# Optimization experiments

Measured on AMD Instinct MI355X. Metric: run time of the kernel, lower is better.

## Reference

```python
import jax, jax.numpy as jnp
import numpy as np

N_NODES = 50000


def sage_conv(x, src, dst, W_l, W_r, b):
    # mean-aggregate neighbor features: out_i = W_l @ mean_{j->i} x_j + W_r @ x_i + b
    msg_sum = jax.ops.segment_sum(x[src], dst, num_segments=N_NODES)   # [N, F]
    cnt = jax.ops.segment_sum(jnp.ones_like(dst, dtype=x.dtype), dst, num_segments=N_NODES)
    mean = msg_sum / jnp.maximum(cnt, 1.0)[:, None]                    # zero for isolated nodes
    return mean @ W_l + x @ W_r + b


def setup_inputs() -> dict:
    key = jax.random.key(0)
    ks = jax.random.split(key, 8)
    in_dim, hid, out_dim = 128, 128, 128
    x = jax.random.normal(ks[0], (N_NODES, in_dim), dtype=jnp.float32)
    edge_index = jax.random.randint(ks[1], (2, 800000), 0, N_NODES, dtype=jnp.int64)
    s0 = 1.0 / np.sqrt(in_dim)
    s1 = 1.0 / np.sqrt(hid)
    return {
        "x": x,
        "edge_index": edge_index,
        "W_l0": jax.random.uniform(ks[2], (in_dim, hid), jnp.float32, -s0, s0),
        "W_r0": jax.random.uniform(ks[3], (in_dim, hid), jnp.float32, -s0, s0),
        "b0": jnp.zeros((hid,), jnp.float32),
        "W_l1": jax.random.uniform(ks[4], (hid, out_dim), jnp.float32, -s1, s1),
        "W_r1": jax.random.uniform(ks[5], (hid, out_dim), jnp.float32, -s1, s1),
        "b1": jnp.zeros((out_dim,), jnp.float32),
    }


def reference(x, edge_index, W_l0, W_r0, b0, W_l1, W_r1, b1):
    src, dst = edge_index[0], edge_index[1]
    h = sage_conv(x, src, dst, W_l0, W_r0, b0)
    h = jax.nn.relu(h)
    out = sage_conv(h, src, dst, W_l1, W_r1, b1)
    return out
```

## Files before the change

### kernel.cpp

```cpp
#include <hip/hip_runtime.h>

#define FDIM 128

typedef __attribute__((ext_vector_type(4))) float f32x4;
typedef __attribute__((ext_vector_type(8))) short s16x8;
typedef __attribute__((ext_vector_type(4))) short s16x4;

__device__ inline unsigned short f2bf(float f) {
    unsigned u = __builtin_bit_cast(unsigned, f);
    u += 0x7FFFu + ((u >> 16) & 1u);
    return (unsigned short)(u >> 16);
}

__global__ void hist_kernel(const int* __restrict__ dst, int* __restrict__ deg, int E) {
    int e = blockIdx.x * blockDim.x + threadIdx.x;
    if (e < E) atomicAdd(&deg[dst[e]], 1);
}

__global__ void scan1_kernel(const int* __restrict__ deg, int* __restrict__ rp,
                             int* __restrict__ bsum, int N) {
    __shared__ int s[256];
    int i = blockIdx.x * 256 + threadIdx.x;
    int v = (i < N) ? deg[i] : 0;
    s[threadIdx.x] = v;
    __syncthreads();
    for (int off = 1; off < 256; off <<= 1) {
        int t = (threadIdx.x >= off) ? s[threadIdx.x - off] : 0;
        __syncthreads();
        s[threadIdx.x] += t;
        __syncthreads();
    }
    if (i < N) rp[i] = s[threadIdx.x] - v;
    if (threadIdx.x == 255) bsum[blockIdx.x] = s[255];
}

__global__ void scan2_kernel(int* __restrict__ bsum, int nb) {
    __shared__ int s[256];
    int v = (threadIdx.x < (unsigned)nb) ? bsum[threadIdx.x] : 0;
    s[threadIdx.x] = v;
    __syncthreads();
    for (int off = 1; off < 256; off <<= 1) {
        int t = (threadIdx.x >= off) ? s[threadIdx.x - off] : 0;
        __syncthreads();
        s[threadIdx.x] += t;
        __syncthreads();
    }
    if (threadIdx.x < (unsigned)nb) bsum[threadIdx.x] = s[threadIdx.x] - v;
}

__global__ void scan3_kernel(int* __restrict__ rp, const int* __restrict__ bsum,
                             int* __restrict__ cursor, int N, int E) {
    int i = blockIdx.x * 256 + threadIdx.x;
    if (i < N) {
        int v = rp[i] + bsum[blockIdx.x];
        rp[i] = v;
        cursor[i] = v;
    } else if (i == N) {
        rp[N] = E;
    }
}

__global__ void fill_kernel(const int* __restrict__ src, const int* __restrict__ dst,
                            int* __restrict__ cursor, int* __restrict__ eid, int E) {
    int e = blockIdx.x * blockDim.x + threadIdx.x;
    if (e < E) {
        int p = atomicAdd(&cursor[dst[e]], 1);
        eid[p] = src[e];
    }
}

__global__ void prep_x_kernel(const float* __restrict__ x, short* __restrict__ xb, int n4) {
    int i = blockIdx.x * blockDim.x + threadIdx.x;
    if (i < n4) {
        float4 v = reinterpret_cast<const float4*>(x)[i];
        s16x4 o;
        o[0] = (short)f2bf(v.x); o[1] = (short)f2bf(v.y);
        o[2] = (short)f2bf(v.z); o[3] = (short)f2bf(v.w);
        reinterpret_cast<s16x4*>(xb)[i] = o;
    }
}

__global__ void prep_w_kernel(const float* __restrict__ Wl0, const float* __restrict__ Wr0,
                              const float* __restrict__ Wl1, const float* __restrict__ Wr1,
                              short* __restrict__ Wt0, short* __restrict__ Wt1) {
    int g = blockIdx.x * blockDim.x + threadIdx.x;
    int n = g & 127;
    int k = (g >> 7) & 255;
    int layer = g >> 15;
    const float* Wl = layer ? Wl1 : Wl0;
    const float* Wr = layer ? Wr1 : Wr0;
    short* Wt = layer ? Wt1 : Wt0;
    float v = (k < 128) ? Wl[k * 128 + n] : Wr[(k - 128) * 128 + n];
    Wt[n * 256 + k] = (short)f2bf(v);
}

__global__ void gather_kernel(const short* __restrict__ xb, const int* __restrict__ rp,
                              const int* __restrict__ eid, short* __restrict__ mb, int N) {
    int node = blockIdx.x * (blockDim.x >> 6) + (threadIdx.x >> 6);
    int lane = threadIdx.x & 63;
    if (node >= N) return;
    int beg = rp[node], end = rp[node + 1];
    float ax = 0.f, ay = 0.f;
    int k = beg;
    for (; k + 4 <= end; k += 4) {
        int s0 = eid[k], s1 = eid[k + 1], s2 = eid[k + 2], s3 = eid[k + 3];
        unsigned u0 = reinterpret_cast<const unsigned*>(xb + (size_t)s0 * FDIM)[lane];
        unsigned u1 = reinterpret_cast<const unsigned*>(xb + (size_t)s1 * FDIM)[lane];
        unsigned u2 = reinterpret_cast<const unsigned*>(xb + (size_t)s2 * FDIM)[lane];
        unsigned u3 = reinterpret_cast<const unsigned*>(xb + (size_t)s3 * FDIM)[lane];
        ax += __builtin_bit_cast(float, u0 << 16) + __builtin_bit_cast(float, u1 << 16)
            + __builtin_bit_cast(float, u2 << 16) + __builtin_bit_cast(float, u3 << 16);
        ay += __builtin_bit_cast(float, u0 & 0xFFFF0000u) + __builtin_bit_cast(float, u1 & 0xFFFF0000u)
            + __builtin_bit_cast(float, u2 & 0xFFFF0000u) + __builtin_bit_cast(float, u3 & 0xFFFF0000u);
    }
    for (; k < end; ++k) {
        int s = eid[k];
        unsigned u = reinterpret_cast<const unsigned*>(xb + (size_t)s * FDIM)[lane];
        ax += __builtin_bit_cast(float, u << 16);
        ay += __builtin_bit_cast(float, u & 0xFFFF0000u);
    }
    float inv = (end > beg) ? 1.0f / (float)(end - beg) : 0.0f;
    unsigned lo = f2bf(ax * inv), hi = f2bf(ay * inv);
    reinterpret_cast<unsigned*>(mb + (size_t)node * FDIM)[lane] = lo | (hi << 16);
}

template <bool RELU, bool OUTF32>
__global__ __launch_bounds__(256, 2)
void gemm_mfma_kernel(const short* __restrict__ Am, const short* Ax,
                      const short* __restrict__ Wt, const float* __restrict__ bias,
                      float* outf, short* outb, int n) {
    __shared__ short A_lds[64 * 256];
    const int tid = threadIdx.x;
    const int w = tid >> 6, l = tid & 63;
    const int row0 = blockIdx.x * 64;

    s16x8 bfr[8][2];
    {
        const short* wb = Wt + ((32 * w + (l & 15)) * 256 + 8 * (l >> 4));
#pragma unroll
        for (int kc = 0; kc < 8; ++kc)
#pragma unroll
            for (int cf = 0; cf < 2; ++cf)
                bfr[kc][cf] = *reinterpret_cast<const s16x8*>(wb + cf * 16 * 256 + kc * 32);
    }

#pragma unroll
    for (int i = 0; i < 8; ++i) {
        int c = tid + 256 * i;
        int r = c >> 5;
        int ck = c & 31;
        int row = row0 + r;
        s16x8 v;
        if (row < n) {
            const short* sp = (ck < 16) ? (Am + (size_t)row * FDIM + ck * 8)
                                        : (Ax + (size_t)row * FDIM + (ck - 16) * 8);
            v = *reinterpret_cast<const s16x8*>(sp);
        } else {
#pragma unroll
            for (int j = 0; j < 8; ++j) v[j] = 0;
        }
        int byte = r * 512 + ((ck * 16) ^ ((r & 7) << 4));
        *reinterpret_cast<s16x8*>(reinterpret_cast<char*>(A_lds) + byte) = v;
    }
    __syncthreads();

    f32x4 acc[4][2];
    {
        float b0 = bias[32 * w + (l & 15)];
        float b1 = bias[32 * w + 16 + (l & 15)];
#pragma unroll
        for (int rf = 0; rf < 4; ++rf)
#pragma unroll
            for (int i = 0; i < 4; ++i) { acc[rf][0][i] = b0; acc[rf][1][i] = b1; }
    }

    const int arow = l & 15;
    const int aq16 = 16 * (l >> 4);
#pragma unroll
    for (int kc = 0; kc < 8; ++kc) {
        s16x8 afr[4];
#pragma unroll
        for (int rf = 0; rf < 4; ++rf) {
            int r = 16 * rf + arow;
            int kbyte = 64 * kc + aq16;
            int byte = r * 512 + (kbyte ^ ((r & 7) << 4));
            afr[rf] = *reinterpret_cast<const s16x8*>(reinterpret_cast<const char*>(A_lds) + byte);
        }
#pragma unroll
        for (int rf = 0; rf < 4; ++rf)
#pragma unroll
            for (int cf = 0; cf < 2; ++cf)
                acc[rf][cf] = __builtin_amdgcn_mfma_f32_16x16x32_bf16(afr[rf], bfr[kc][cf], acc[rf][cf], 0, 0, 0);
    }

    const int ocol = 32 * w + (l & 15);
    const int orow = 4 * (l >> 4);
#pragma unroll
    for (int rf = 0; rf < 4; ++rf)
#pragma unroll
        for (int cf = 0; cf < 2; ++cf)
#pragma unroll
            for (int i = 0; i < 4; ++i) {
                int row = row0 + 16 * rf + orow + i;
                if (row < n) {
                    float v = acc[rf][cf][i];
                    if (RELU) v = fmaxf(v, 0.0f);
                    if (OUTF32) outf[(size_t)row * FDIM + ocol + 16 * cf] = v;
                    else        outb[(size_t)row * FDIM + ocol + 16 * cf] = (short)f2bf(v);
                }
            }
}

__global__ void degree_kernel(const int* __restrict__ dst, float* __restrict__ cnt, int E) {
    int e = blockIdx.x * blockDim.x + threadIdx.x;
    if (e < E) atomicAdd(&cnt[dst[e]], 1.0f);
}

__global__ void scatter_kernel(const float* __restrict__ x, const int* __restrict__ src,
                               const int* __restrict__ dst, float* __restrict__ msg, int E) {
    int gt = blockIdx.x * blockDim.x + threadIdx.x;
    int e = gt >> 6;
    int lane = gt & 63;
    if (e >= E) return;
    int s = src[e];
    int d = dst[e];
    float2 v = reinterpret_cast<const float2*>(x + (size_t)s * FDIM)[lane];
    float* md = msg + (size_t)d * FDIM + 2 * lane;
    atomicAdd(md, v.x);
    atomicAdd(md + 1, v.y);
}

template <bool RELU>
__global__ void gemm_kernel(const float* agg, const float* cnt,
                            const float* __restrict__ xin, const float* __restrict__ Wl,
                            const float* __restrict__ Wr, const float* __restrict__ bias,
                            float* out, int n) {
    const int ROWS = 16;
    __shared__ float m_s[ROWS][FDIM];
    __shared__ float x_s[ROWS][FDIM];
    int tid = threadIdx.x;
    int row0 = blockIdx.x * ROWS;
#pragma unroll
    for (int i = 0; i < 2; ++i) {
        int idx4 = tid + i * 256;
        int r = idx4 >> 5;
        int c4 = idx4 & 31;
        int row = row0 + r;
        if (row < n) {
            float inv = cnt ? 1.0f / fmaxf(cnt[row], 1.0f) : 1.0f;
            float4 mv = reinterpret_cast<const float4*>(agg + (size_t)row * FDIM)[c4];
            float4 xv = reinterpret_cast<const float4*>(xin + (size_t)row * FDIM)[c4];
            float* mp = &m_s[r][c4 * 4];
            mp[0] = mv.x * inv; mp[1] = mv.y * inv; mp[2] = mv.z * inv; mp[3] = mv.w * inv;
            float* xp = &x_s[r][c4 * 4];
            xp[0] = xv.x; xp[1] = xv.y; xp[2] = xv.z; xp[3] = xv.w;
        }
    }
    __syncthreads();
    int j = tid & 127;
    int rh = tid >> 7;
    float acc[8];
    float bj = bias[j];
#pragma unroll
    for (int r = 0; r < 8; ++r) acc[r] = bj;
#pragma unroll 4
    for (int k = 0; k < FDIM; ++k) {
        float wl = Wl[k * FDIM + j];
        float wr = Wr[k * FDIM + j];
#pragma unroll
        for (int r = 0; r < 8; ++r)
            acc[r] += m_s[rh * 8 + r][k] * wl + x_s[rh * 8 + r][k] * wr;
    }
#pragma unroll
    for (int r = 0; r < 8; ++r) {
        int row = row0 + rh * 8 + r;
        if (row < n) {
            float v = acc[r];
            if (RELU) v = fmaxf(v, 0.0f);
            out[(size_t)row * FDIM + j] = v;
        }
    }
}

extern "C" void kernel_launch(void* const* d_in, const int* in_sizes, int n_in,
                              void* d_out, int out_size, void* d_ws, size_t ws_size,
                              hipStream_t stream) {
    const float* x   = (const float*)d_in[0];
    const int*   ei  = (const int*)d_in[1];
    const float* Wl0 = (const float*)d_in[2];
    const float* Wr0 = (const float*)d_in[3];
    const float* b0  = (const float*)d_in[4];
    const float* Wl1 = (const float*)d_in[5];
    const float* Wr1 = (const float*)d_in[6];
    const float* b1  = (const float*)d_in[7];

    int N = in_sizes[0] / FDIM;
    int E = in_sizes[1] / 2;
    const int* src = ei;
    const int* dst = ei + E;

    size_t featBytes  = (size_t)N * FDIM * sizeof(float);
    size_t featBytesB = (size_t)N * FDIM * sizeof(short);
    int edgeBlocks = (E + 255) / 256;
    int nb = (N + 255) / 256;

    const size_t o_deg  = 0;
    const size_t o_rp   = 0x40000;
    const size_t o_cur  = 0x80000;
    const size_t o_bsum = 0xC0000;
    const size_t o_wt0  = 0xD0000;
    const size_t o_wt1  = 0xE0000;
    const size_t o_eid  = 0x100000;
    const size_t o_xb   = 0x440000;
    const size_t o_mb   = o_xb + featBytesB;
    const size_t need   = o_mb + featBytesB;

    if (ws_size >= need) {
        int*   deg    = (int*)((char*)d_ws + o_deg);
        int*   rp     = (int*)((char*)d_ws + o_rp);
        int*   cursor = (int*)((char*)d_ws + o_cur);
        int*   bsum   = (int*)((char*)d_ws + o_bsum);
        short* Wt0    = (short*)((char*)d_ws + o_wt0);
        short* Wt1    = (short*)((char*)d_ws + o_wt1);
        int*   eid    = (int*)((char*)d_ws + o_eid);
        short* xb     = (short*)((char*)d_ws + o_xb);
        short* mb     = (short*)((char*)d_ws + o_mb);
        float* outF   = (float*)d_out;

        hipMemsetAsync(deg, 0, (size_t)N * sizeof(int), stream);
        hist_kernel<<<edgeBlocks, 256, 0, stream>>>(dst, deg, E);
        scan1_kernel<<<nb, 256, 0, stream>>>(deg, rp, bsum, N);
        scan2_kernel<<<1, 256, 0, stream>>>(bsum, nb);
        scan3_kernel<<<(N + 256) / 256, 256, 0, stream>>>(rp, bsum, cursor, N, E);
        fill_kernel<<<edgeBlocks, 256, 0, stream>>>(src, dst, cursor, eid, E);

        prep_w_kernel<<<256, 256, 0, stream>>>(Wl0, Wr0, Wl1, Wr1, Wt0, Wt1);
        prep_x_kernel<<<(N * FDIM / 4 + 255) / 256, 256, 0, stream>>>(x, xb, N * FDIM / 4);

        int gatherBlocks = (N + 3) / 4;
        int gemmBlocks   = (N + 63) / 64;
        gather_kernel<<<gatherBlocks, 256, 0, stream>>>(xb, rp, eid, mb, N);
        gemm_mfma_kernel<true, false><<<gemmBlocks, 256, 0, stream>>>(mb, xb, Wt0, b0, nullptr, xb, N);
        gather_kernel<<<gatherBlocks, 256, 0, stream>>>(xb, rp, eid, mb, N);
        gemm_mfma_kernel<false, true><<<gemmBlocks, 256, 0, stream>>>(mb, xb, Wt1, b1, outF, nullptr, N);
    } else {
        float* cnt = (float*)d_ws;
        float* h   = (float*)((char*)d_ws + (1 << 18));
        float* msg = (float*)d_out;
        int gemmBlocks = (N + 15) / 16;

        hipMemsetAsync(cnt, 0, (size_t)N * sizeof(float), stream);
        degree_kernel<<<edgeBlocks, 256, 0, stream>>>(dst, cnt, E);

        hipMemsetAsync(msg, 0, featBytes, stream);
        scatter_kernel<<<(E * 64 + 255) / 256, 256, 0, stream>>>(x, src, dst, msg, E);
        gemm_kernel<true><<<gemmBlocks, 256, 0, stream>>>(msg, cnt, x, Wl0, Wr0, b0, h, N);

        hipMemsetAsync(msg, 0, featBytes, stream);
        scatter_kernel<<<(E * 64 + 255) / 256, 256, 0, stream>>>(h, src, dst, msg, E);
        gemm_kernel<false><<<gemmBlocks, 256, 0, stream>>>(msg, cnt, h, Wl1, Wr1, b1, msg, N);
    }
}
```

Before: 218.0 us.

## Fuse neighbor mean-gather into MFMA GEMM kernel, writing aggregates directly to LDS

Merges the separate gather and GEMM kernels per layer into one kernel. Each wave gathers 16 rows of neighbor means straight into the swizzled LDS A tile, next to the self features, and then runs the MFMA GEMM. This removes the intermediate mean buffer round trip through global memory and two launches per layer, and it unrolls the gather by 8 for more loads in flight. A separate output buffer is now used for layer 1 because the kernel reads X for neighbors. In exchange, only 4 waves per 64 rows do the latency-bound gather, with fewer blocks than the old gather launch. Occupancy is raised to 3 blocks/SM via launch bounds to compensate.

```diff
diff --git a/kernel.cpp b/kernel.cpp
--- a/kernel.cpp
+++ b/kernel.cpp
@@ -11,6 +11,8 @@
     u += 0x7FFFu + ((u >> 16) & 1u);
     return (unsigned short)(u >> 16);
 }
+__device__ inline float bflo(unsigned u) { return __builtin_bit_cast(float, u << 16); }
+__device__ inline float bfhi(unsigned u) { return __builtin_bit_cast(float, u & 0xFFFF0000u); }
 
 __global__ void hist_kernel(const int* __restrict__ dst, int* __restrict__ deg, int E) {
     int e = blockIdx.x * blockDim.x + threadIdx.x;
@@ -94,46 +96,69 @@
     Wt[n * 256 + k] = (short)f2bf(v);
 }
 
-__global__ void gather_kernel(const short* __restrict__ xb, const int* __restrict__ rp,
-                              const int* __restrict__ eid, short* __restrict__ mb, int N) {
-    int node = blockIdx.x * (blockDim.x >> 6) + (threadIdx.x >> 6);
-    int lane = threadIdx.x & 63;
-    if (node >= N) return;
-    int beg = rp[node], end = rp[node + 1];
-    float ax = 0.f, ay = 0.f;
-    int k = beg;
-    for (; k + 4 <= end; k += 4) {
-        int s0 = eid[k], s1 = eid[k + 1], s2 = eid[k + 2], s3 = eid[k + 3];
-        unsigned u0 = reinterpret_cast<const unsigned*>(xb + (size_t)s0 * FDIM)[lane];
-        unsigned u1 = reinterpret_cast<const unsigned*>(xb + (size_t)s1 * FDIM)[lane];
-        unsigned u2 = reinterpret_cast<const unsigned*>(xb + (size_t)s2 * FDIM)[lane];
-        unsigned u3 = reinterpret_cast<const unsigned*>(xb + (size_t)s3 * FDIM)[lane];
-        ax += __builtin_bit_cast(float, u0 << 16) + __builtin_bit_cast(float, u1 << 16)
-            + __builtin_bit_cast(float, u2 << 16) + __builtin_bit_cast(float, u3 << 16);
-        ay += __builtin_bit_cast(float, u0 & 0xFFFF0000u) + __builtin_bit_cast(float, u1 & 0xFFFF0000u)
-            + __builtin_bit_cast(float, u2 & 0xFFFF0000u) + __builtin_bit_cast(float, u3 & 0xFFFF0000u);
-    }
-    for (; k < end; ++k) {
-        int s = eid[k];
-        unsigned u = reinterpret_cast<const unsigned*>(xb + (size_t)s * FDIM)[lane];
-        ax += __builtin_bit_cast(float, u << 16);
-        ay += __builtin_bit_cast(float, u & 0xFFFF0000u);
-    }
-    float inv = (end > beg) ? 1.0f / (float)(end - beg) : 0.0f;
-    unsigned lo = f2bf(ax * inv), hi = f2bf(ay * inv);
-    reinterpret_cast<unsigned*>(mb + (size_t)node * FDIM)[lane] = lo | (hi << 16);
-}
-
 template <bool RELU, bool OUTF32>
-__global__ __launch_bounds__(256, 2)
-void gemm_mfma_kernel(const short* __restrict__ Am, const short* Ax,
-                      const short* __restrict__ Wt, const float* __restrict__ bias,
-                      float* outf, short* outb, int n) {
+__global__ __launch_bounds__(256, 3)
+void fused_kernel(const short* __restrict__ X, const int* __restrict__ rp,
+                  const int* __restrict__ eid, const short* __restrict__ Wt,
+                  const float* __restrict__ bias, float* outf, short* outb, int n) {
     __shared__ short A_lds[64 * 256];
     const int tid = threadIdx.x;
     const int w = tid >> 6, l = tid & 63;
     const int row0 = blockIdx.x * 64;
 
+#pragma unroll
+    for (int i = 0; i < 4; ++i) {
+        int c = tid + 256 * i;
+        int r = c >> 4;
+        int ck = c & 15;
+        int row = row0 + r;
+        s16x8 v;
+        if (row < n) {
+            v = *reinterpret_cast<const s16x8*>(X + (size_t)row * FDIM + ck * 8);
+        } else {
+#pragma unroll
+            for (int j = 0; j < 8; ++j) v[j] = 0;
+        }
+        int byte = r * 512 + ((256 + ck * 16) ^ ((r & 7) << 4));
+        *reinterpret_cast<s16x8*>(reinterpret_cast<char*>(A_lds) + byte) = v;
+    }
+
+    for (int rr = 0; rr < 16; ++rr) {
+        int r = 16 * w + rr;
+        int row = row0 + r;
+        float ax = 0.f, ay = 0.f;
+        int beg = 0, end = 0;
+        if (row < n) { beg = rp[row]; end = rp[row + 1]; }
+        int k = beg;
+        for (; k + 8 <= end; k += 8) {
+            unsigned u[8];
+#pragma unroll
+            for (int q = 0; q < 8; ++q) {
+                int s = eid[k + q];
+                u[q] = reinterpret_cast<const unsigned*>(X + (size_t)s * FDIM)[l];
+            }
+#pragma unroll
+            for (int q = 0; q < 8; ++q) { ax += bflo(u[q]); ay += bfhi(u[q]); }
+        }
+        for (; k + 2 <= end; k += 2) {
+            int s0 = eid[k], s1 = eid[k + 1];
+            unsigned u0 = reinterpret_cast<const unsigned*>(X + (size_t)s0 * FDIM)[l];
+            unsigned u1 = reinterpret_cast<const unsigned*>(X + (size_t)s1 * FDIM)[l];
+            ax += bflo(u0) + bflo(u1);
+            ay += bfhi(u0) + bfhi(u1);
+        }
+        for (; k < end; ++k) {
+            int s = eid[k];
+            unsigned u = reinterpret_cast<const unsigned*>(X + (size_t)s * FDIM)[l];
+            ax += bflo(u);
+            ay += bfhi(u);
+        }
+        float inv = (end > beg) ? 1.0f / (float)(end - beg) : 0.0f;
+        unsigned lo = f2bf(ax * inv), hi = f2bf(ay * inv);
+        int byte = r * 512 + ((4 * l) ^ ((r & 7) << 4));
+        *reinterpret_cast<unsigned*>(reinterpret_cast<char*>(A_lds) + byte) = lo | (hi << 16);
+    }
+
     s16x8 bfr[8][2];
     {
         const short* wb = Wt + ((32 * w + (l & 15)) * 256 + 8 * (l >> 4));
@@ -144,24 +169,6 @@
                 bfr[kc][cf] = *reinterpret_cast<const s16x8*>(wb + cf * 16 * 256 + kc * 32);
     }
 
-#pragma unroll
-    for (int i = 0; i < 8; ++i) {
-        int c = tid + 256 * i;
-        int r = c >> 5;
-        int ck = c & 31;
-        int row = row0 + r;
-        s16x8 v;
-        if (row < n) {
-            const short* sp = (ck < 16) ? (Am + (size_t)row * FDIM + ck * 8)
-                                        : (Ax + (size_t)row * FDIM + (ck - 16) * 8);
-            v = *reinterpret_cast<const s16x8*>(sp);
-        } else {
-#pragma unroll
-            for (int j = 0; j < 8; ++j) v[j] = 0;
-        }
-        int byte = r * 512 + ((ck * 16) ^ ((r & 7) << 4));
-        *reinterpret_cast<s16x8*>(reinterpret_cast<char*>(A_lds) + byte) = v;
-    }
     __syncthreads();
 
     f32x4 acc[4][2];
@@ -312,8 +319,8 @@
     const size_t o_wt1  = 0xE0000;
     const size_t o_eid  = 0x100000;
     const size_t o_xb   = 0x440000;
-    const size_t o_mb   = o_xb + featBytesB;
-    const size_t need   = o_mb + featBytesB;
+    const size_t o_hb   = o_xb + featBytesB;
+    const size_t need   = o_hb + featBytesB;
 
     if (ws_size >= need) {
         int*   deg    = (int*)((char*)d_ws + o_deg);
@@ -324,7 +331,7 @@
         short* Wt1    = (short*)((char*)d_ws + o_wt1);
         int*   eid    = (int*)((char*)d_ws + o_eid);
         short* xb     = (short*)((char*)d_ws + o_xb);
-        short* mb     = (short*)((char*)d_ws + o_mb);
+        short* hb     = (short*)((char*)d_ws + o_hb);
         float* outF   = (float*)d_out;
 
         hipMemsetAsync(deg, 0, (size_t)N * sizeof(int), stream);
@@ -337,12 +344,9 @@
         prep_w_kernel<<<256, 256, 0, stream>>>(Wl0, Wr0, Wl1, Wr1, Wt0, Wt1);
         prep_x_kernel<<<(N * FDIM / 4 + 255) / 256, 256, 0, stream>>>(x, xb, N * FDIM / 4);
 
-        int gatherBlocks = (N + 3) / 4;
-        int gemmBlocks   = (N + 63) / 64;
-        gather_kernel<<<gatherBlocks, 256, 0, stream>>>(xb, rp, eid, mb, N);
-        gemm_mfma_kernel<true, false><<<gemmBlocks, 256, 0, stream>>>(mb, xb, Wt0, b0, nullptr, xb, N);
-        gather_kernel<<<gatherBlocks, 256, 0, stream>>>(xb, rp, eid, mb, N);
-        gemm_mfma_kernel<false, true><<<gemmBlocks, 256, 0, stream>>>(mb, xb, Wt1, b1, outF, nullptr, N);
+        int fusedBlocks = (N + 63) / 64;
+        fused_kernel<true, false><<<fusedBlocks, 256, 0, stream>>>(xb, rp, eid, Wt0, b0, nullptr, hb, N);
+        fused_kernel<false, true><<<fusedBlocks, 256, 0, stream>>>(hb, rp, eid, Wt1, b1, outF, nullptr, N);
     } else {
         float* cnt = (float*)d_ws;
         float* h   = (float*)((char*)d_ws + (1 << 18));
```

Result: slower. 237.6 us (+9.0%).

## Two-phase binned CSR fill with LDS cursors and wider gather unroll

Applied to the files above, without the earlier changes.

Replaces the per-edge global atomic CSR fill with a two-pass scheme. First, edges are staged into bins keyed by 128-node destination partition and a block sub-bin. A second kernel then places them using LDS cursor atomics, with an overflow fallback to the old global path. The staging buffer reuses the mb region before it is needed. The gather loop is also unrolled to 8 neighbors to keep more loads in flight. This adds an extra kernel and a round trip through staging memory.

```diff
diff --git a/kernel.cpp b/kernel.cpp
--- a/kernel.cpp
+++ b/kernel.cpp
@@ -1,6 +1,7 @@
 #include <hip/hip_runtime.h>
 
 #define FDIM 128
+#define BIN_CAP 500
 
 typedef __attribute__((ext_vector_type(4))) float f32x4;
 typedef __attribute__((ext_vector_type(8))) short s16x8;
@@ -11,6 +12,8 @@
     u += 0x7FFFu + ((u >> 16) & 1u);
     return (unsigned short)(u >> 16);
 }
+__device__ inline float bflo(unsigned u) { return __builtin_bit_cast(float, u << 16); }
+__device__ inline float bfhi(unsigned u) { return __builtin_bit_cast(float, u & 0xFFFF0000u); }
 
 __global__ void hist_kernel(const int* __restrict__ dst, int* __restrict__ deg, int E) {
     int e = blockIdx.x * blockDim.x + threadIdx.x;
@@ -60,12 +63,42 @@
     }
 }
 
-__global__ void fill_kernel(const int* __restrict__ src, const int* __restrict__ dst,
+__global__ void binA_kernel(const int* __restrict__ src, const int* __restrict__ dst,
+                            int* __restrict__ pcur, int2* __restrict__ stag,
                             int* __restrict__ cursor, int* __restrict__ eid, int E) {
     int e = blockIdx.x * blockDim.x + threadIdx.x;
-    if (e < E) {
-        int p = atomicAdd(&cursor[dst[e]], 1);
-        eid[p] = src[e];
+    if (e >= E) return;
+    int d = dst[e], s = src[e];
+    int bin = (d >> 7) * 8 + (blockIdx.x & 7);
+    int slot = atomicAdd(&pcur[bin], 1);
+    if (slot < BIN_CAP) {
+        stag[(size_t)bin * BIN_CAP + slot] = make_int2(s, d);
+    } else {
+        int p = atomicAdd(&cursor[d], 1);
+        eid[p] = s;
+    }
+}
+
+__global__ void binB_kernel(const int* __restrict__ pcur, const int2* __restrict__ stag,
+                            const int* __restrict__ cursor, int* __restrict__ eid, int N) {
+    __shared__ int lcur[128];
+    int part = blockIdx.x;
+    int node0 = part << 7;
+    if (threadIdx.x < 128) {
+        int node = node0 + threadIdx.x;
+        lcur[threadIdx.x] = (node < N) ? cursor[node] : 0;
+    }
+    __syncthreads();
+#pragma unroll
+    for (int g = 0; g < 8; ++g) {
+        int bin = part * 8 + g;
+        int cnt = min(pcur[bin], BIN_CAP);
+        const int2* base = stag + (size_t)bin * BIN_CAP;
+        for (int i = threadIdx.x; i < cnt; i += 256) {
+            int2 sd = base[i];
+            int p = atomicAdd(&lcur[sd.y & 127], 1);
+            eid[p] = sd.x;
+        }
     }
 }
 
@@ -102,22 +135,28 @@
     int beg = rp[node], end = rp[node + 1];
     float ax = 0.f, ay = 0.f;
     int k = beg;
-    for (; k + 4 <= end; k += 4) {
-        int s0 = eid[k], s1 = eid[k + 1], s2 = eid[k + 2], s3 = eid[k + 3];
+    for (; k + 8 <= end; k += 8) {
+        unsigned u[8];
+#pragma unroll
+        for (int q = 0; q < 8; ++q) {
+            int s = eid[k + q];
+            u[q] = reinterpret_cast<const unsigned*>(xb + (size_t)s * FDIM)[lane];
+        }
+#pragma unroll
+        for (int q = 0; q < 8; ++q) { ax += bflo(u[q]); ay += bfhi(u[q]); }
+    }
+    for (; k + 2 <= end; k += 2) {
+        int s0 = eid[k], s1 = eid[k + 1];
         unsigned u0 = reinterpret_cast<const unsigned*>(xb + (size_t)s0 * FDIM)[lane];
         unsigned u1 = reinterpret_cast<const unsigned*>(xb + (size_t)s1 * FDIM)[lane];
-        unsigned u2 = reinterpret_cast<const unsigned*>(xb + (size_t)s2 * FDIM)[lane];
-        unsigned u3 = reinterpret_cast<const unsigned*>(xb + (size_t)s3 * FDIM)[lane];
-        ax += __builtin_bit_cast(float, u0 << 16) + __builtin_bit_cast(float, u1 << 16)
-            + __builtin_bit_cast(float, u2 << 16) + __builtin_bit_cast(float, u3 << 16);
-        ay += __builtin_bit_cast(float, u0 & 0xFFFF0000u) + __builtin_bit_cast(float, u1 & 0xFFFF0000u)
-            + __builtin_bit_cast(float, u2 & 0xFFFF0000u) + __builtin_bit_cast(float, u3 & 0xFFFF0000u);
+        ax += bflo(u0) + bflo(u1);
+        ay += bfhi(u0) + bfhi(u1);
     }
     for (; k < end; ++k) {
         int s = eid[k];
         unsigned u = reinterpret_cast<const unsigned*>(xb + (size_t)s * FDIM)[lane];
-        ax += __builtin_bit_cast(float, u << 16);
-        ay += __builtin_bit_cast(float, u & 0xFFFF0000u);
+        ax += bflo(u);
+        ay += bfhi(u);
     }
     float inv = (end > beg) ? 1.0f / (float)(end - beg) : 0.0f;
     unsigned lo = f2bf(ax * inv), hi = f2bf(ay * inv);
@@ -303,11 +342,13 @@
     size_t featBytesB = (size_t)N * FDIM * sizeof(short);
     int edgeBlocks = (E + 255) / 256;
     int nb = (N + 255) / 256;
+    int npart = (N + 127) >> 7;
 
     const size_t o_deg  = 0;
     const size_t o_rp   = 0x40000;
     const size_t o_cur  = 0x80000;
     const size_t o_bsum = 0xC0000;
+    const size_t o_pcur = 0xC4000;
     const size_t o_wt0  = 0xD0000;
     const size_t o_wt1  = 0xE0000;
     const size_t o_eid  = 0x100000;
@@ -315,24 +356,30 @@
     const size_t o_mb   = o_xb + featBytesB;
     const size_t need   = o_mb + featBytesB;
 
-    if (ws_size >= need) {
+    bool stag_fits = (size_t)npart * 8 * BIN_CAP * sizeof(int2) <= featBytesB;
+
+    if (ws_size >= need && stag_fits) {
         int*   deg    = (int*)((char*)d_ws + o_deg);
         int*   rp     = (int*)((char*)d_ws + o_rp);
         int*   cursor = (int*)((char*)d_ws + o_cur);
         int*   bsum   = (int*)((char*)d_ws + o_bsum);
+        int*   pcur   = (int*)((char*)d_ws + o_pcur);
         short* Wt0    = (short*)((char*)d_ws + o_wt0);
         short* Wt1    = (short*)((char*)d_ws + o_wt1);
         int*   eid    = (int*)((char*)d_ws + o_eid);
         short* xb     = (short*)((char*)d_ws + o_xb);
         short* mb     = (short*)((char*)d_ws + o_mb);
+        int2*  stag   = (int2*)((char*)d_ws + o_mb);
         float* outF   = (float*)d_out;
 
         hipMemsetAsync(deg, 0, (size_t)N * sizeof(int), stream);
+        hipMemsetAsync(pcur, 0, (size_t)npart * 8 * sizeof(int), stream);
         hist_kernel<<<edgeBlocks, 256, 0, stream>>>(dst, deg, E);
         scan1_kernel<<<nb, 256, 0, stream>>>(deg, rp, bsum, N);
         scan2_kernel<<<1, 256, 0, stream>>>(bsum, nb);
         scan3_kernel<<<(N + 256) / 256, 256, 0, stream>>>(rp, bsum, cursor, N, E);
-        fill_kernel<<<edgeBlocks, 256, 0, stream>>>(src, dst, cursor, eid, E);
+        binA_kernel<<<edgeBlocks, 256, 0, stream>>>(src, dst, pcur, stag, cursor, eid, E);
+        binB_kernel<<<npart, 256, 0, stream>>>(pcur, stag, cursor, eid, N);
 
         prep_w_kernel<<<256, 256, 0, stream>>>(Wl0, Wr0, Wl1, Wr1, Wt0, Wt1);
         prep_x_kernel<<<(N * FDIM / 4 + 255) / 256, 256, 0, stream>>>(x, xb, N * FDIM / 4);
```

Measured after the change: 241.8 us. 1.11x slower.

## Split CSR build into 8 atomic groups and vectorize gather with 16-byte loads

Applied to the files above, without the earlier changes.

The CSR construction now keeps eight separate degree and cursor arrays, chosen by block index, to spread atomic contention. It then scans them jointly, derives row pointers, fills a temporary edge array and merges the groups back into per-node order. The gather kernel now has each wavefront process four edges at once: each group of 16 lanes loads 16-byte bf16 chunks, and the partial sums are reduced with cross-lane shuffles. The price is extra kernels, an 8x larger count array to clear, scan and read, and a serial per-thread merge loop.

```diff
diff --git a/kernel.cpp b/kernel.cpp
--- a/kernel.cpp
+++ b/kernel.cpp
@@ -1,6 +1,7 @@
 #include <hip/hip_runtime.h>
 
 #define FDIM 128
+#define NGRP 8
 
 typedef __attribute__((ext_vector_type(4))) float f32x4;
 typedef __attribute__((ext_vector_type(8))) short s16x8;
@@ -11,18 +12,29 @@
     u += 0x7FFFu + ((u >> 16) & 1u);
     return (unsigned short)(u >> 16);
 }
-
-__global__ void hist_kernel(const int* __restrict__ dst, int* __restrict__ deg, int E) {
+__device__ inline float bflo(unsigned u) { return __builtin_bit_cast(float, u << 16); }
+__device__ inline float bfhi(unsigned u) { return __builtin_bit_cast(float, u & 0xFFFF0000u); }
+
+
+__global__ void hist8_kernel(const int* __restrict__ dst, int* __restrict__ degg, int E, int N) {
     int e = blockIdx.x * blockDim.x + threadIdx.x;
-    if (e < E) atomicAdd(&deg[dst[e]], 1);
-}
-
-__global__ void scan1_kernel(const int* __restrict__ deg, int* __restrict__ rp,
-                             int* __restrict__ bsum, int N) {
+    if (e < E) atomicAdd(&degg[(blockIdx.x & 7) * N + dst[e]], 1);
+}
+
+__global__ void scanA1_kernel(const int* __restrict__ in, int* __restrict__ out,
+                              int* __restrict__ bsum, int M) {
     __shared__ int s[256];
-    int i = blockIdx.x * 256 + threadIdx.x;
-    int v = (i < N) ? deg[i] : 0;
-    s[threadIdx.x] = v;
+    int base = blockIdx.x * 1024 + threadIdx.x * 4;
+    int4 v = make_int4(0, 0, 0, 0);
+    if (base + 3 < M) v = *reinterpret_cast<const int4*>(in + base);
+    else {
+        if (base + 0 < M) v.x = in[base + 0];
+        if (base + 1 < M) v.y = in[base + 1];
+        if (base + 2 < M) v.z = in[base + 2];
+        if (base + 3 < M) v.w = in[base + 3];
+    }
+    int tsum = v.x + v.y + v.z + v.w;
+    s[threadIdx.x] = tsum;
     __syncthreads();
     for (int off = 1; off < 256; off <<= 1) {
         int t = (threadIdx.x >= off) ? s[threadIdx.x - off] : 0;
@@ -30,16 +42,24 @@
         s[threadIdx.x] += t;
         __syncthreads();
     }
-    if (i < N) rp[i] = s[threadIdx.x] - v;
+    int excl = s[threadIdx.x] - tsum;
+    int4 o;
+    o.x = excl; o.y = excl + v.x; o.z = o.y + v.y; o.w = o.z + v.z;
+    if (base + 3 < M) *reinterpret_cast<int4*>(out + base) = o;
+    else {
+        if (base + 0 < M) out[base + 0] = o.x;
+        if (base + 1 < M) out[base + 1] = o.y;
+        if (base + 2 < M) out[base + 2] = o.z;
+    }
     if (threadIdx.x == 255) bsum[blockIdx.x] = s[255];
 }
 
-__global__ void scan2_kernel(int* __restrict__ bsum, int nb) {
-    __shared__ int s[256];
+__global__ void scanA2_kernel(int* __restrict__ bsum, int nb) {
+    __shared__ int s[512];
     int v = (threadIdx.x < (unsigned)nb) ? bsum[threadIdx.x] : 0;
     s[threadIdx.x] = v;
     __syncthreads();
-    for (int off = 1; off < 256; off <<= 1) {
+    for (int off = 1; off < 512; off <<= 1) {
         int t = (threadIdx.x >= off) ? s[threadIdx.x - off] : 0;
         __syncthreads();
         s[threadIdx.x] += t;
@@ -48,24 +68,62 @@
     if (threadIdx.x < (unsigned)nb) bsum[threadIdx.x] = s[threadIdx.x] - v;
 }
 
-__global__ void scan3_kernel(int* __restrict__ rp, const int* __restrict__ bsum,
-                             int* __restrict__ cursor, int N, int E) {
+__global__ void scanA3_kernel(int* __restrict__ off, int* __restrict__ cursor,
+                              const int* __restrict__ bsum, int M, int E) {
+    int base = blockIdx.x * 1024 + threadIdx.x * 4;
+    int b = bsum[blockIdx.x];
+    if (base + 3 < M) {
+        int4 v = *reinterpret_cast<const int4*>(off + base);
+        v.x += b; v.y += b; v.z += b; v.w += b;
+        *reinterpret_cast<int4*>(off + base) = v;
+        *reinterpret_cast<int4*>(cursor + base) = v;
+    } else {
+#pragma unroll
+        for (int j = 0; j < 4; ++j)
+            if (base + j < M) { int t = off[base + j] + b; off[base + j] = t; cursor[base + j] = t; }
+    }
+    if (base == 0) off[M] = E;
+}
+
+__global__ void rp_kernel(const int* __restrict__ off, int* __restrict__ rp, int N, int E) {
+    __shared__ int S0;
+    if (threadIdx.x == 0) {
+        int s = 0;
+#pragma unroll
+        for (int g = 0; g < NGRP; ++g) s += off[g * N];
+        S0 = s;
+    }
+    __syncthreads();
     int i = blockIdx.x * 256 + threadIdx.x;
     if (i < N) {
-        int v = rp[i] + bsum[blockIdx.x];
-        rp[i] = v;
-        cursor[i] = v;
+        int s = 0;
+#pragma unroll
+        for (int g = 0; g < NGRP; ++g) s += off[g * N + i];
+        rp[i] = s - S0;
     } else if (i == N) {
         rp[N] = E;
     }
 }
 
-__global__ void fill_kernel(const int* __restrict__ src, const int* __restrict__ dst,
-                            int* __restrict__ cursor, int* __restrict__ eid, int E) {
+__global__ void fill8_kernel(const int* __restrict__ src, const int* __restrict__ dst,
+                             int* __restrict__ cursor, int* __restrict__ eidt, int E, int N) {
     int e = blockIdx.x * blockDim.x + threadIdx.x;
     if (e < E) {
-        int p = atomicAdd(&cursor[dst[e]], 1);
-        eid[p] = src[e];
+        int p = atomicAdd(&cursor[(blockIdx.x & 7) * N + dst[e]], 1);
+        eidt[p] = src[e];
+    }
+}
+
+__global__ void merge_kernel(const int* __restrict__ off, const int* __restrict__ eidt,
+                             const int* __restrict__ rp, int* __restrict__ eid, int N) {
+    int i = blockIdx.x * 256 + threadIdx.x;
+    if (i >= N) return;
+    int dp = rp[i];
+#pragma unroll
+    for (int g = 0; g < NGRP; ++g) {
+        int b = off[g * N + i];
+        int e2 = off[g * N + i + 1];
+        for (int k = b; k < e2; ++k) eid[dp++] = eidt[k];
     }
 }
 
@@ -94,34 +152,57 @@
     Wt[n * 256 + k] = (short)f2bf(v);
 }
 
-__global__ void gather_kernel(const short* __restrict__ xb, const int* __restrict__ rp,
+#define ACC8(v) { a[0]+=bflo(v.x); a[1]+=bfhi(v.x); a[2]+=bflo(v.y); a[3]+=bfhi(v.y); \
+                  a[4]+=bflo(v.z); a[5]+=bfhi(v.z); a[6]+=bflo(v.w); a[7]+=bfhi(v.w); }
+
+__global__ void gather_kernel(const short* __restrict__ X, const int* __restrict__ rp,
                               const int* __restrict__ eid, short* __restrict__ mb, int N) {
     int node = blockIdx.x * (blockDim.x >> 6) + (threadIdx.x >> 6);
     int lane = threadIdx.x & 63;
+    int g = lane >> 4;
+    int c = lane & 15;
     if (node >= N) return;
     int beg = rp[node], end = rp[node + 1];
-    float ax = 0.f, ay = 0.f;
+    float a[8];
+#pragma unroll
+    for (int j = 0; j < 8; ++j) a[j] = 0.0f;
+
     int k = beg;
-    for (; k + 4 <= end; k += 4) {
-        int s0 = eid[k], s1 = eid[k + 1], s2 = eid[k + 2], s3 = eid[k + 3];
-        unsigned u0 = reinterpret_cast<const unsigned*>(xb + (size_t)s0 * FDIM)[lane];
-        unsigned u1 = reinterpret_cast<const unsigned*>(xb + (size_t)s1 * FDIM)[lane];
-        unsigned u2 = reinterpret_cast<const unsigned*>(xb + (size_t)s2 * FDIM)[lane];
-        unsigned u3 = reinterpret_cast<const unsigned*>(xb + (size_t)s3 * FDIM)[lane];
-        ax += __builtin_bit_cast(float, u0 << 16) + __builtin_bit_cast(float, u1 << 16)
-            + __builtin_bit_cast(float, u2 << 16) + __builtin_bit_cast(float, u3 << 16);
-        ay += __builtin_bit_cast(float, u0 & 0xFFFF0000u) + __builtin_bit_cast(float, u1 & 0xFFFF0000u)
-            + __builtin_bit_cast(float, u2 & 0xFFFF0000u) + __builtin_bit_cast(float, u3 & 0xFFFF0000u);
-    }
-    for (; k < end; ++k) {
-        int s = eid[k];
-        unsigned u = reinterpret_cast<const unsigned*>(xb + (size_t)s * FDIM)[lane];
-        ax += __builtin_bit_cast(float, u << 16);
-        ay += __builtin_bit_cast(float, u & 0xFFFF0000u);
-    }
-    float inv = (end > beg) ? 1.0f / (float)(end - beg) : 0.0f;
-    unsigned lo = f2bf(ax * inv), hi = f2bf(ay * inv);
-    reinterpret_cast<unsigned*>(mb + (size_t)node * FDIM)[lane] = lo | (hi << 16);
+    for (; k + 8 <= end; k += 8) {
+        int s0 = eid[k + g];
+        int s1 = eid[k + 4 + g];
+        uint4 v0 = *reinterpret_cast<const uint4*>(X + (size_t)s0 * FDIM + c * 8);
+        uint4 v1 = *reinterpret_cast<const uint4*>(X + (size_t)s1 * FDIM + c * 8);
+        ACC8(v0);
+        ACC8(v1);
+    }
+    if (k + 4 <= end) {
+        int s0 = eid[k + g];
+        uint4 v0 = *reinterpret_cast<const uint4*>(X + (size_t)s0 * FDIM + c * 8);
+        ACC8(v0);
+        k += 4;
+    }
+    int rem = end - k;
+    if (g < rem) {
+        int s0 = eid[k + g];
+        uint4 v0 = *reinterpret_cast<const uint4*>(X + (size_t)s0 * FDIM + c * 8);
+        ACC8(v0);
+    }
+
+#pragma unroll
+    for (int j = 0; j < 8; ++j) a[j] += __shfl_xor(a[j], 16);
+#pragma unroll
+    for (int j = 0; j < 8; ++j) a[j] += __shfl_xor(a[j], 32);
+
+    if (g == 0) {
+        float inv = (end > beg) ? 1.0f / (float)(end - beg) : 0.0f;
+        uint4 o;
+        o.x = (unsigned)f2bf(a[0] * inv) | ((unsigned)f2bf(a[1] * inv) << 16);
+        o.y = (unsigned)f2bf(a[2] * inv) | ((unsigned)f2bf(a[3] * inv) << 16);
+        o.z = (unsigned)f2bf(a[4] * inv) | ((unsigned)f2bf(a[5] * inv) << 16);
+        o.w = (unsigned)f2bf(a[6] * inv) | ((unsigned)f2bf(a[7] * inv) << 16);
+        *reinterpret_cast<uint4*>(mb + (size_t)node * FDIM + c * 8) = o;
+    }
 }
 
 template <bool RELU, bool OUTF32>
@@ -302,37 +383,44 @@
     size_t featBytes  = (size_t)N * FDIM * sizeof(float);
     size_t featBytesB = (size_t)N * FDIM * sizeof(short);
     int edgeBlocks = (E + 255) / 256;
-    int nb = (N + 255) / 256;
-
-    const size_t o_deg  = 0;
-    const size_t o_rp   = 0x40000;
-    const size_t o_cur  = 0x80000;
-    const size_t o_bsum = 0xC0000;
-    const size_t o_wt0  = 0xD0000;
-    const size_t o_wt1  = 0xE0000;
-    const size_t o_eid  = 0x100000;
-    const size_t o_xb   = 0x440000;
+    int M = NGRP * N;
+    int blocksA = (M + 1023) / 1024;
+
+    const size_t o_bsum = 0x0;
+    const size_t o_rp   = 0x1000;
+    const size_t o_wt0  = 0x33000;
+    const size_t o_wt1  = 0x43000;
+    const size_t o_eid  = 0x53000;
+    const size_t o_xb   = 0x361000;
     const size_t o_mb   = o_xb + featBytesB;
     const size_t need   = o_mb + featBytesB;
+    const size_t s_degg = o_mb + 0x0;
+    const size_t s_off  = o_mb + 0x187000;
+    const size_t s_cur  = o_mb + 0x30E000;
+    const size_t s_eidt = o_mb + 0x495000;
 
     if (ws_size >= need) {
-        int*   deg    = (int*)((char*)d_ws + o_deg);
+        int*   bsum   = (int*)((char*)d_ws + o_bsum);
         int*   rp     = (int*)((char*)d_ws + o_rp);
-        int*   cursor = (int*)((char*)d_ws + o_cur);
-        int*   bsum   = (int*)((char*)d_ws + o_bsum);
         short* Wt0    = (short*)((char*)d_ws + o_wt0);
         short* Wt1    = (short*)((char*)d_ws + o_wt1);
         int*   eid    = (int*)((char*)d_ws + o_eid);
         short* xb     = (short*)((char*)d_ws + o_xb);
         short* mb     = (short*)((char*)d_ws + o_mb);
+        int*   degg   = (int*)((char*)d_ws + s_degg);
+        int*   off    = (int*)((char*)d_ws + s_off);
+        int*   cursor = (int*)((char*)d_ws + s_cur);
+        int*   eidt   = (int*)((char*)d_ws + s_eidt);
         float* outF   = (float*)d_out;
 
-        hipMemsetAsync(deg, 0, (size_t)N * sizeof(int), stream);
-        hist_kernel<<<edgeBlocks, 256, 0, stream>>>(dst, deg, E);
-        scan1_kernel<<<nb, 256, 0, stream>>>(deg, rp, bsum, N);
-        scan2_kernel<<<1, 256, 0, stream>>>(bsum, nb);
-        scan3_kernel<<<(N + 256) / 256, 256, 0, stream>>>(rp, bsum, cursor, N, E);
-        fill_kernel<<<edgeBlocks, 256, 0, stream>>>(src, dst, cursor, eid, E);
+        hipMemsetAsync(degg, 0, (size_t)M * sizeof(int), stream);
+        hist8_kernel<<<edgeBlocks, 256, 0, stream>>>(dst, degg, E, N);
+        scanA1_kernel<<<blocksA, 256, 0, stream>>>(degg, off, bsum, M);
+        scanA2_kernel<<<1, 512, 0, stream>>>(bsum, blocksA);
+        scanA3_kernel<<<blocksA, 256, 0, stream>>>(off, cursor, bsum, M, E);
+        rp_kernel<<<(N + 256) / 256, 256, 0, stream>>>(off, rp, N, E);
+        fill8_kernel<<<edgeBlocks, 256, 0, stream>>>(src, dst, cursor, eidt, E, N);
+        merge_kernel<<<(N + 255) / 256, 256, 0, stream>>>(off, eidt, rp, eid, N);
 
         prep_w_kernel<<<256, 256, 0, stream>>>(Wl0, Wr0, Wl1, Wr1, Wt0, Wt1);
         prep_x_kernel<<<(N * FDIM / 4 + 255) / 256, 256, 0, stream>>>(x, xb, N * FDIM / 4);
```

Measured after the change: 199.3 us. 8.6% less time.
